# Performance work log

Measured on AMD Instinct MI355X. Metric: run time of the kernel, lower is better.

The kernel has to match this reference:

```python
import jax, jax.numpy as jnp
import numpy as np

B, S, SEG, D = 2, 128, 128, 768
RL, H, DK = 16, 8, 64
DV = D // H            # 96, dim_value = dim // heads
NRPF = D // H          # num_rel_pos_features
N = S * RL             # 2048 attention tokens
SCALE = DK ** -0.5


def setup_inputs() -> dict:
    key = jax.random.key(0)
    ks = jax.random.split(key, 12)
    g = lambda k, sh: jax.random.normal(k, sh, jnp.float32) * 0.02
    return {
        'x': jax.random.normal(ks[0], (B, S, SEG, D), jnp.float32),
        'ln_g': jnp.ones((D,), jnp.float32),
        'ln_b': jnp.zeros((D,), jnp.float32),
        'Wq': g(ks[1], (D, H * DK)),
        'Wk': g(ks[2], (D, H * DK)),
        'Wv': g(ks[3], (D, H * DV)),
        'Wr': g(ks[4], (NRPF, H * DK)),
        'r_w_bias': g(ks[5], (H, DK)),
        'r_r_bias': g(ks[6], (H, DK)),
        'Wo': g(ks[7], (H * DV, D)),
        'bo': jnp.zeros((D,), jnp.float32),
        'pos_emb': g(ks[8], (2 * N - 1, NRPF)),  # relative position features, dist -(N-1)..(N-1)
    }


def _layernorm(x, g, b, eps=1e-5):
    mu = jnp.mean(x, -1, keepdims=True)
    var = jnp.var(x, -1, keepdims=True)
    return (x - mu) * jax.lax.rsqrt(var + eps) * g + b


def _relative_shift(t):
    # t: [b, h, n, 2n-1] -> [b, h, n, n] (enformer-style shift)
    b, h, n, _ = t.shape
    t = jnp.pad(t, ((0, 0), (0, 0), (0, 0), (1, 0)))      # [b,h,n,2n]
    t = t.reshape(b, h, 2 * n, n)[:, :, 1:, :]            # [b,h,2n-1,n]
    t = t.reshape(b, h, n, 2 * n - 1)
    return t[..., :n]


def reference(x, ln_g, ln_b, Wq, Wk, Wv, Wr, r_w_bias, r_r_bias, Wo, bo, pos_emb):
    # slice representative tokens per segment and flatten: b s n d -> b (s n) d
    reps = x[:, :, :RL, :].reshape(B, N, D)
    h = _layernorm(reps, ln_g, ln_b)
    q = (h @ Wq).reshape(B, N, H, DK).transpose(0, 2, 1, 3) * SCALE  # bhnd
    k = (h @ Wk).reshape(B, N, H, DK).transpose(0, 2, 1, 3)
    v = (h @ Wv).reshape(B, N, H, DV).transpose(0, 2, 1, 3)
    content = jnp.einsum('bhid,bhjd->bhij', q + r_w_bias[None, :, None, :], k)
    rel_k = (pos_emb @ Wr).reshape(2 * N - 1, H, DK)
    rel = jnp.einsum('bhid,rhd->bhir', q + r_r_bias[None, :, None, :], rel_k)
    logits = content + _relative_shift(rel)
    attn = jax.nn.softmax(logits, axis=-1)
    out = jnp.einsum('bhij,bhjd->bhid', attn, v)
    out = out.transpose(0, 2, 1, 3).reshape(B, N, H * DV) @ Wo + bo
    reps = (reps + out).reshape(B, S, RL, D)  # residual transformer block, un-flatten
    return jnp.concatenate([reps, x[:, :, RL:, :]], axis=2)
```

## Files before the change

kernel.cpp:

```cpp
#include <hip/hip_runtime.h>

typedef short s8v __attribute__((ext_vector_type(8)));
typedef float f4 __attribute__((ext_vector_type(4)));

__device__ inline float bf2f(unsigned short u) {
  union { unsigned i; float f; } x; x.i = (unsigned)u << 16; return x.f;
}
__device__ inline unsigned short f2bf(float f) {
  union { float f; unsigned i; } x; x.f = f;
  return (unsigned short)((x.i + 0x7fffu + ((x.i >> 16) & 1u)) >> 16);
}

__device__ inline void gload16(const void* g, void* l) {
  __builtin_amdgcn_global_load_lds(
      (const __attribute__((address_space(1))) unsigned int*)g,
      (__attribute__((address_space(3))) unsigned int*)l, 16, 0, 0);
}

__device__ inline void bar_lgkm() {
  asm volatile("s_waitcnt lgkmcnt(0)" ::: "memory");
  __builtin_amdgcn_s_barrier();
  asm volatile("" ::: "memory");
}

__global__ __launch_bounds__(256) void copy4(const float4* __restrict__ src,
                                             float4* __restrict__ dst, int n4) {
  int i = blockIdx.x * blockDim.x + threadIdx.x;
  int stride = gridDim.x * blockDim.x;
  for (; i < n4; i += stride) dst[i] = src[i];
}

__global__ __launch_bounds__(256) void ln_kernel(const float* __restrict__ x,
                                                 const float* __restrict__ g,
                                                 const float* __restrict__ bvec,
                                                 unsigned short* __restrict__ h) {
  int m = blockIdx.x;
  int b = m >> 11, n = m & 2047;
  int s = n >> 4, rl = n & 15;
  const float* row = x + ((size_t)((b * 128 + s) * 128 + rl)) * 768;
  int t = threadIdx.x;
  float v0 = row[t], v1 = row[t + 256], v2 = row[t + 512];
  float sum = v0 + v1 + v2;
  float sq = v0 * v0 + v1 * v1 + v2 * v2;
  __shared__ float rs[4], rq[4];
#pragma unroll
  for (int o = 32; o; o >>= 1) {
    sum += __shfl_down(sum, o);
    sq += __shfl_down(sq, o);
  }
  if ((t & 63) == 0) { rs[t >> 6] = sum; rq[t >> 6] = sq; }
  __syncthreads();
  sum = rs[0] + rs[1] + rs[2] + rs[3];
  sq = rq[0] + rq[1] + rq[2] + rq[3];
  float mu = sum * (1.f / 768.f);
  float var = sq * (1.f / 768.f) - mu * mu;
  float inv = rsqrtf(var + 1e-5f);
  unsigned short* hrow = h + (size_t)m * 768;
  hrow[t] = f2bf((v0 - mu) * inv * g[t] + bvec[t]);
  hrow[t + 256] = f2bf((v1 - mu) * inv * g[t + 256] + bvec[t + 256]);
  hrow[t + 512] = f2bf((v2 - mu) * inv * g[t + 512] + bvec[t + 512]);
}

__global__ __launch_bounds__(256) void transp_cvt(const float* __restrict__ Wq,
                                                  const float* __restrict__ Wk,
                                                  const float* __restrict__ Wv,
                                                  const float* __restrict__ Wo,
                                                  unsigned short* __restrict__ Bt,
                                                  unsigned short* __restrict__ Bto) {
  int z = blockIdx.z;
  const float* src; unsigned short* dst; int N;
  if (z == 0) { src = Wq; dst = Bt; N = 512; }
  else if (z == 1) { src = Wk; dst = Bt + (size_t)512 * 768; N = 512; }
  else if (z == 2) { src = Wv; dst = Bt + (size_t)1024 * 768; N = 768; }
  else { src = Wo; dst = Bto; N = 768; }
  int n0 = blockIdx.x << 6, k0 = blockIdx.y << 6;
  if (n0 >= N) return;
  __shared__ float tile[64][65];
  int t = threadIdx.x;
  int c4 = (t & 15) << 2, rr = t >> 4;
#pragma unroll
  for (int i = 0; i < 4; ++i) {
    int kr = rr + (i << 4);
    float4 v = *(const float4*)(src + (size_t)(k0 + kr) * N + n0 + c4);
    tile[c4 + 0][kr] = v.x; tile[c4 + 1][kr] = v.y;
    tile[c4 + 2][kr] = v.z; tile[c4 + 3][kr] = v.w;
  }
  __syncthreads();
  int rowN = t >> 2, kc = (t & 3) << 4;
#pragma unroll
  for (int j = 0; j < 16; ++j)
    dst[(size_t)(n0 + rowN) * 768 + k0 + kc + j] = f2bf(tile[rowN][kc + j]);
}

__global__ __launch_bounds__(256) void gemm_rel(const float* __restrict__ A,
                                                const float* __restrict__ Bw,
                                                unsigned short* __restrict__ C0,
                                                int M, int Nn, int K) {
  __shared__ float As[16][68];
  __shared__ float Bs[16][68];
  int t = threadIdx.x;
  int tx = t & 15, ty = t >> 4;
  int row0 = blockIdx.y << 6, col0 = blockIdx.x << 6;
  float acc[4][4] = {{0.f}};
  int ar = t >> 2, ac = (t & 3) << 2;
  int br = t >> 4, bc = (t & 15) << 2;
  for (int k0 = 0; k0 < K; k0 += 16) {
    float4 av = make_float4(0.f, 0.f, 0.f, 0.f);
    if (row0 + ar < M) av = *(const float4*)(A + (size_t)(row0 + ar) * K + k0 + ac);
    As[ac + 0][ar] = av.x; As[ac + 1][ar] = av.y;
    As[ac + 2][ar] = av.z; As[ac + 3][ar] = av.w;
    float4 bv = *(const float4*)(Bw + (size_t)(k0 + br) * Nn + col0 + bc);
    *(float4*)&Bs[br][bc] = bv;
    __syncthreads();
#pragma unroll
    for (int kk = 0; kk < 16; ++kk) {
      float4 a = *(const float4*)&As[kk][ty << 2];
      float4 b = *(const float4*)&Bs[kk][tx << 2];
      float arr[4] = {a.x, a.y, a.z, a.w};
      float brr[4] = {b.x, b.y, b.z, b.w};
#pragma unroll
      for (int i = 0; i < 4; ++i)
#pragma unroll
        for (int j = 0; j < 4; ++j) acc[i][j] += arr[i] * brr[j];
    }
    __syncthreads();
  }
#pragma unroll
  for (int i = 0; i < 4; ++i) {
    int r = row0 + (ty << 2) + i;
    if (r >= M) continue;
    int colb = col0 + (tx << 2);
    unsigned pk0 = f2bf(acc[i][0]) | ((unsigned)f2bf(acc[i][1]) << 16);
    unsigned pk1 = f2bf(acc[i][2]) | ((unsigned)f2bf(acc[i][3]) << 16);
    *(uint2*)(C0 + (size_t)r * Nn + colb) = make_uint2(pk0, pk1);
  }
}

template <int MODE>
__global__ __launch_bounds__(256) void gemm_mfma(
    const unsigned short* __restrict__ A, const unsigned short* __restrict__ Bt,
    unsigned short* __restrict__ qw, unsigned short* __restrict__ qr,
    unsigned short* __restrict__ kbuf, unsigned short* __restrict__ vt,
    const float* __restrict__ rwb, const float* __restrict__ rrb,
    const float* __restrict__ x, const float* __restrict__ bo,
    float* __restrict__ out) {
  __shared__ __align__(16) short As[128 * 64];
  __shared__ __align__(16) short Bs[128 * 64];
  const int t = threadIdx.x;
  const int w = t >> 6, lane = t & 63;
  const int m16 = lane & 15, quad = lane >> 4;
  const int wm = w >> 1, wn = w & 1;
  const int m0 = blockIdx.y << 7, n0 = blockIdx.x << 7;
  const int K = 768;

  f4 acc[4][4];
#pragma unroll
  for (int i = 0; i < 4; ++i)
#pragma unroll
    for (int j = 0; j < 4; ++j) acc[i][j] = (f4){0.f, 0.f, 0.f, 0.f};

  const int rA = lane >> 3;
  const int cA = lane & 7;

  for (int k0 = 0; k0 < K; k0 += 64) {
    __syncthreads();
#pragma unroll
    for (int i = 0; i < 4; ++i) {
      int seg = (w << 2) + i;
      int r = (seg << 3) + rA;
      int cg = cA ^ (r & 7);
      gload16(A + (size_t)(m0 + r) * K + k0 + (cg << 3), (short*)As + (seg << 9));
      gload16(Bt + (size_t)(n0 + r) * K + k0 + (cg << 3), (short*)Bs + (seg << 9));
    }
    __syncthreads();
#pragma unroll
    for (int kb = 0; kb < 2; ++kb) {
      int cs = ((kb << 2) + quad) ^ (m16 & 7);
      s8v af[4], bf[4];
#pragma unroll
      for (int mt = 0; mt < 4; ++mt) {
        int r = (wm << 6) + (mt << 4) + m16;
        af[mt] = *(const s8v*)(As + (r << 6) + (cs << 3));
      }
#pragma unroll
      for (int nt = 0; nt < 4; ++nt) {
        int rn = (wn << 6) + (nt << 4) + m16;
        bf[nt] = *(const s8v*)(Bs + (rn << 6) + (cs << 3));
      }
#pragma unroll
      for (int mt = 0; mt < 4; ++mt)
#pragma unroll
        for (int nt = 0; nt < 4; ++nt)
          acc[mt][nt] = __builtin_amdgcn_mfma_f32_16x16x32_bf16(af[mt], bf[nt], acc[mt][nt], 0, 0, 0);
    }
  }

#pragma unroll
  for (int nt = 0; nt < 4; ++nt) {
    int n = n0 + (wn << 6) + (nt << 4) + m16;
#pragma unroll
    for (int mt = 0; mt < 4; ++mt) {
#pragma unroll
      for (int rr = 0; rr < 4; ++rr) {
        int m = m0 + (wm << 6) + (mt << 4) + (quad << 2) + rr;
        float v = acc[mt][nt][rr];
        if (MODE == 0) {
          if (n < 512) {
            float vs = v * 0.125f;
            qw[(size_t)m * 512 + n] = f2bf(vs + rwb[n]);
            qr[(size_t)m * 512 + n] = f2bf(vs + rrb[n]);
          } else if (n < 1024) {
            kbuf[(size_t)m * 512 + (n - 512)] = f2bf(v);
          } else {
            int col = n - 1024;
            int b = m >> 11, j = m & 2047;
            vt[(((size_t)(b * 768 + col)) << 11) + j] = f2bf(v);
          }
        } else {
          int b = m >> 11, nn2 = m & 2047;
          int s = nn2 >> 4, rl = nn2 & 15;
          size_t base = ((size_t)((b * 128 + s) * 128 + rl)) * 768;
          out[base + n] = x[base + n] + v + bo[n];
        }
      }
    }
  }
}

__global__ __launch_bounds__(256) void attn_kernel(
    const unsigned short* __restrict__ qw_g, const unsigned short* __restrict__ qr_g,
    const unsigned short* __restrict__ k_g, const unsigned short* __restrict__ vt_g,
    const unsigned short* __restrict__ rk_g, unsigned short* __restrict__ ao) {
  const int qt = blockIdx.x, hh = blockIdx.y, b = blockIdx.z;
  const int i0 = qt << 5;
  const int t = threadIdx.x;
  const int lane = t & 63, w = t >> 6;
  const int m16 = lane & 15, quad = lane >> 4;
  const int mi = w & 1, njb = w >> 1;
  const int sr = t >> 3, sg = t & 7;

  __shared__ __align__(16) short qw_s[32 * 64];
  __shared__ __align__(16) short qr_s[32 * 64];
  __shared__ __align__(16) short k_s[2][64 * 64];
  __shared__ __align__(16) short rk_s[2][96 * 64];
  __shared__ __align__(16) short pb_s[32 * 64];
  __shared__ float p_s[32][68];
  __shared__ short t_s[32][104];
  __shared__ float alpha_s[32];
  __shared__ float linv_s[32];

  for (int u = t; u < 512; u += 256) {
    int tile = u >> 8, idx = u & 255, r = idx >> 3, ch = idx & 7;
    const unsigned short* src =
        (tile ? qr_g : qw_g) + (((size_t)(b * 2048 + i0 + r)) << 9) + (hh << 6) + (ch << 3);
    int4 vdat = *(const int4*)src;
    short* dst = (tile ? qr_s : qw_s) + r * 64 + (((ch ^ (r & 7))) << 3);
    *(int4*)dst = vdat;
  }

  {
    const int rb0 = 2016 - i0;
#pragma unroll
    for (int s = 0; s < 2; ++s) {
      int slot = w * 2 + s;
      int u = (slot << 6) + lane;
      int r = u >> 3, c = u & 7;
      int cg = c ^ (r & 7);
      gload16(k_g + (((size_t)(b * 2048 + r)) << 9) + (hh << 6) + (cg << 3),
              (short*)k_s[0] + (slot << 9));
    }
#pragma unroll
    for (int s = 0; s < 3; ++s) {
      int slot = w * 3 + s;
      int u = (slot << 6) + lane;
      int r = u >> 3, c = u & 7;
      int cg = c ^ (r & 7);
      int grow = rb0 + r; if (grow > 4094) grow = 4094;
      gload16(rk_g + (((size_t)grow) << 9) + (hh << 6) + (cg << 3),
              (short*)rk_s[0] + (slot << 9));
    }
  }
  __syncthreads();

  float m_i = -1e30f, l_i = 0.f;
  f4 o0 = {0.f, 0.f, 0.f, 0.f}, o1 = o0, o2 = o0;
  const int arow = mi * 16 + m16;
  const int asw = arow & 7;
  const int crow = mi * 16 + quad * 4;
  const int brow0 = njb * 16 + m16;
  const int bsw = brow0 & 7;

  const unsigned short* vbase = vt_g + (((size_t)(b * 768 + hh * 96 + brow0)) << 11);

  for (int j0 = 0; j0 < 2048; j0 += 64) {
    const int cur = (j0 >> 6) & 1;

    const unsigned short* vb = vbase + j0;
    s8v va0 = *(const s8v*)(vb + (quad << 3));
    s8v va1 = *(const s8v*)(vb + 65536 + (quad << 3));
    s8v va2 = *(const s8v*)(vb + 131072 + (quad << 3));
    s8v vc0 = *(const s8v*)(vb + ((4 + quad) << 3));
    s8v vc1 = *(const s8v*)(vb + 65536 + ((4 + quad) << 3));
    s8v vc2 = *(const s8v*)(vb + 131072 + ((4 + quad) << 3));

    if (j0 < 1984) {
      const int j0n = j0 + 64;
      const int rbn = 2016 + j0n - i0;
#pragma unroll
      for (int s = 0; s < 2; ++s) {
        int slot = w * 2 + s;
        int u = (slot << 6) + lane;
        int r = u >> 3, c = u & 7;
        int cg = c ^ (r & 7);
        gload16(k_g + (((size_t)(b * 2048 + j0n + r)) << 9) + (hh << 6) + (cg << 3),
                (short*)k_s[cur ^ 1] + (slot << 9));
      }
#pragma unroll
      for (int s = 0; s < 3; ++s) {
        int slot = w * 3 + s;
        int u = (slot << 6) + lane;
        int r = u >> 3, c = u & 7;
        int cg = c ^ (r & 7);
        int grow = rbn + r; if (grow > 4094) grow = 4094;
        gload16(rk_g + (((size_t)grow) << 9) + (hh << 6) + (cg << 3),
                (short*)rk_s[cur ^ 1] + (slot << 9));
      }
    }

    if (j0 < 1984) asm volatile("s_waitcnt vmcnt(11)" ::: "memory");
    else           asm volatile("s_waitcnt vmcnt(6)" ::: "memory");
    __builtin_amdgcn_sched_barrier(0);

    const short* ks = k_s[cur];
    const short* rs = rk_s[cur];
    f4 c0 = {0.f, 0.f, 0.f, 0.f}, c1 = c0;
    f4 r0 = c0, r1 = c0, r2 = c0;
#pragma unroll
    for (int kb = 0; kb < 2; ++kb) {
      const int cidx = (kb << 2) + quad;
      const int co = (cidx ^ asw) << 3;
      const int cb = (cidx ^ bsw) << 3;
      s8v aq = *(const s8v*)(qw_s + arow * 64 + co);
      s8v ar = *(const s8v*)(qr_s + arow * 64 + co);
      s8v bk0 = *(const s8v*)(ks + brow0 * 64 + cb);
      s8v bk1 = *(const s8v*)(ks + (brow0 + 32) * 64 + cb);
      s8v br0 = *(const s8v*)(rs + brow0 * 64 + cb);
      s8v br1 = *(const s8v*)(rs + (brow0 + 32) * 64 + cb);
      s8v br2 = *(const s8v*)(rs + (brow0 + 64) * 64 + cb);
      __builtin_amdgcn_s_setprio(1);
      c0 = __builtin_amdgcn_mfma_f32_16x16x32_bf16(aq, bk0, c0, 0, 0, 0);
      c1 = __builtin_amdgcn_mfma_f32_16x16x32_bf16(aq, bk1, c1, 0, 0, 0);
      r0 = __builtin_amdgcn_mfma_f32_16x16x32_bf16(ar, br0, r0, 0, 0, 0);
      r1 = __builtin_amdgcn_mfma_f32_16x16x32_bf16(ar, br1, r1, 0, 0, 0);
      r2 = __builtin_amdgcn_mfma_f32_16x16x32_bf16(ar, br2, r2, 0, 0, 0);
      __builtin_amdgcn_s_setprio(0);
    }
#pragma unroll
    for (int rr = 0; rr < 4; ++rr) {
      p_s[crow + rr][njb * 16 + m16] = c0[rr];
      p_s[crow + rr][(njb + 2) * 16 + m16] = c1[rr];
      t_s[crow + rr][njb * 16 + m16] = (short)f2bf(r0[rr]);
      t_s[crow + rr][(njb + 2) * 16 + m16] = (short)f2bf(r1[rr]);
      t_s[crow + rr][(njb + 4) * 16 + m16] = (short)f2bf(r2[rr]);
    }
    bar_lgkm();

    float sv[8];
    float mx = -1e30f;
#pragma unroll
    for (int j2 = 0; j2 < 8; ++j2) {
      int c = sg + (j2 << 3);
      float s = p_s[sr][c] + bf2f((unsigned short)t_s[sr][c - sr + 31]);
      sv[j2] = s;
      mx = fmaxf(mx, s);
    }
    mx = fmaxf(mx, __shfl_xor(mx, 1));
    mx = fmaxf(mx, __shfl_xor(mx, 2));
    mx = fmaxf(mx, __shfl_xor(mx, 4));
    float m_new = fmaxf(m_i, mx);
    float al = __expf(m_i - m_new);
    float sm = 0.f;
#pragma unroll
    for (int j2 = 0; j2 < 8; ++j2) {
      float p = __expf(sv[j2] - m_new);
      sm += p;
      pb_s[sr * 64 + ((j2 ^ (sr & 7)) << 3) + sg] = (short)f2bf(p);
    }
    sm += __shfl_xor(sm, 1);
    sm += __shfl_xor(sm, 2);
    sm += __shfl_xor(sm, 4);
    l_i = l_i * al + sm;
    m_i = m_new;
    if (sg == 0) alpha_s[sr] = al;
    bar_lgkm();

#pragma unroll
    for (int rr = 0; rr < 4; ++rr) {
      float a = alpha_s[crow + rr];
      o0[rr] *= a; o1[rr] *= a; o2[rr] *= a;
    }
#pragma unroll
    for (int kb = 0; kb < 2; ++kb) {
      const int cidx = (kb << 2) + quad;
      const int co = (cidx ^ asw) << 3;
      s8v ap = *(const s8v*)(pb_s + arow * 64 + co);
      s8v b0v = kb ? vc0 : va0;
      s8v b1v = kb ? vc1 : va1;
      s8v b2v = kb ? vc2 : va2;
      __builtin_amdgcn_s_setprio(1);
      o0 = __builtin_amdgcn_mfma_f32_16x16x32_bf16(ap, b0v, o0, 0, 0, 0);
      o1 = __builtin_amdgcn_mfma_f32_16x16x32_bf16(ap, b1v, o1, 0, 0, 0);
      o2 = __builtin_amdgcn_mfma_f32_16x16x32_bf16(ap, b2v, o2, 0, 0, 0);
      __builtin_amdgcn_s_setprio(0);
    }
  }

  if (sg == 0) linv_s[sr] = 1.f / l_i;
  __syncthreads();
#pragma unroll
  for (int rr = 0; rr < 4; ++rr) {
    int row = crow + rr;
    float inv = linv_s[row];
    size_t gbase = ((size_t)(b * 2048 + i0 + row)) * 768 + hh * 96;
    ao[gbase + njb * 16 + m16] = f2bf(o0[rr] * inv);
    ao[gbase + (njb + 2) * 16 + m16] = f2bf(o1[rr] * inv);
    ao[gbase + (njb + 4) * 16 + m16] = f2bf(o2[rr] * inv);
  }
}

extern "C" void kernel_launch(void* const* d_in, const int* in_sizes, int n_in,
                              void* d_out, int out_size, void* d_ws, size_t ws_size,
                              hipStream_t stream) {
  (void)in_sizes; (void)n_in; (void)out_size; (void)ws_size;
  const float* x = (const float*)d_in[0];
  const float* ln_g = (const float*)d_in[1];
  const float* ln_b = (const float*)d_in[2];
  const float* Wq = (const float*)d_in[3];
  const float* Wk = (const float*)d_in[4];
  const float* Wv = (const float*)d_in[5];
  const float* Wr = (const float*)d_in[6];
  const float* rwb = (const float*)d_in[7];
  const float* rrb = (const float*)d_in[8];
  const float* Wo = (const float*)d_in[9];
  const float* bo = (const float*)d_in[10];
  const float* pe = (const float*)d_in[11];
  float* out = (float*)d_out;

  char* p = (char*)d_ws;
  unsigned short* hbf = (unsigned short*)p; p += (size_t)4096 * 768 * 2;
  unsigned short* qw = (unsigned short*)p;  p += (size_t)4096 * 512 * 2;
  unsigned short* qr = (unsigned short*)p;  p += (size_t)4096 * 512 * 2;
  unsigned short* kb = (unsigned short*)p;  p += (size_t)4096 * 512 * 2;
  unsigned short* vt = (unsigned short*)p;  p += (size_t)4096 * 768 * 2;
  unsigned short* rk = (unsigned short*)p;  p += (size_t)4095 * 512 * 2;
  unsigned short* ao = (unsigned short*)p;  p += (size_t)4096 * 768 * 2;
  unsigned short* Bt = (unsigned short*)p;  p += (size_t)1792 * 768 * 2;
  unsigned short* Bto = (unsigned short*)p;

  transp_cvt<<<dim3(12, 12, 4), dim3(256), 0, stream>>>(Wq, Wk, Wv, Wo, Bt, Bto);
  copy4<<<dim3(2048), dim3(256), 0, stream>>>((const float4*)x, (float4*)out, 6291456);
  ln_kernel<<<dim3(4096), dim3(256), 0, stream>>>(x, ln_g, ln_b, hbf);
  gemm_rel<<<dim3(8, 64), dim3(256), 0, stream>>>(pe, Wr, rk, 4095, 512, 96);
  gemm_mfma<0><<<dim3(14, 32), dim3(256), 0, stream>>>(hbf, Bt, qw, qr, kb, vt, rwb, rrb,
                                                       nullptr, nullptr, nullptr);
  attn_kernel<<<dim3(64, 8, 2), dim3(256), 0, stream>>>(qw, qr, kb, vt, rk, ao);
  gemm_mfma<1><<<dim3(6, 32), dim3(256), 0, stream>>>(ao, Bto, nullptr, nullptr, nullptr,
                                                      nullptr, nullptr, nullptr, x, bo, out);
}
```

Before: 410.0 us.

## Fuse output copy into attention kernel and keep rel-pos keys in registers

Removes the standalone copy kernel and spreads the x-to-out copy across the first 24 iterations of the attention loop, so memory traffic overlaps MFMA work. Relative-position key fragments are now loaded directly from global memory into registers, with a one-iteration prefetch, instead of being staged in LDS. This cuts shared memory use, and occupancy is requested at 3 blocks per SM. The tradeoffs are higher register pressure, global loads that are not coalesced through LDS, and a hand-tuned vmcnt wait that must stay correct.

```diff
diff --git a/kernel.cpp b/kernel.cpp
--- a/kernel.cpp
+++ b/kernel.cpp
@@ -21,13 +21,6 @@
   asm volatile("s_waitcnt lgkmcnt(0)" ::: "memory");
   __builtin_amdgcn_s_barrier();
   asm volatile("" ::: "memory");
-}
-
-__global__ __launch_bounds__(256) void copy4(const float4* __restrict__ src,
-                                             float4* __restrict__ dst, int n4) {
-  int i = blockIdx.x * blockDim.x + threadIdx.x;
-  int stride = gridDim.x * blockDim.x;
-  for (; i < n4; i += stride) dst[i] = src[i];
 }
 
 __global__ __launch_bounds__(256) void ln_kernel(const float* __restrict__ x,
@@ -227,10 +220,11 @@
   }
 }
 
-__global__ __launch_bounds__(256) void attn_kernel(
+__global__ __launch_bounds__(256, 3) void attn_kernel(
     const unsigned short* __restrict__ qw_g, const unsigned short* __restrict__ qr_g,
     const unsigned short* __restrict__ k_g, const unsigned short* __restrict__ vt_g,
-    const unsigned short* __restrict__ rk_g, unsigned short* __restrict__ ao) {
+    const unsigned short* __restrict__ rk_g, unsigned short* __restrict__ ao,
+    const float4* __restrict__ xc, float4* __restrict__ outc) {
   const int qt = blockIdx.x, hh = blockIdx.y, b = blockIdx.z;
   const int i0 = qt << 5;
   const int t = threadIdx.x;
@@ -238,16 +232,22 @@
   const int m16 = lane & 15, quad = lane >> 4;
   const int mi = w & 1, njb = w >> 1;
   const int sr = t >> 3, sg = t & 7;
+  const int bid = qt + (hh << 6) + (b << 9);
 
   __shared__ __align__(16) short qw_s[32 * 64];
   __shared__ __align__(16) short qr_s[32 * 64];
   __shared__ __align__(16) short k_s[2][64 * 64];
-  __shared__ __align__(16) short rk_s[2][96 * 64];
   __shared__ __align__(16) short pb_s[32 * 64];
   __shared__ float p_s[32][68];
   __shared__ short t_s[32][104];
   __shared__ float alpha_s[32];
   __shared__ float linv_s[32];
+
+  const int arow = mi * 16 + m16;
+  const int asw = arow & 7;
+  const int crow = mi * 16 + quad * 4;
+  const int brow0 = njb * 16 + m16;
+  const int bsw = brow0 & 7;
 
   for (int u = t; u < 512; u += 256) {
     int tile = u >> 8, idx = u & 255, r = idx >> 3, ch = idx & 7;
@@ -258,39 +258,39 @@
     *(int4*)dst = vdat;
   }
 
+#pragma unroll
+  for (int s = 0; s < 2; ++s) {
+    int slot = w * 2 + s;
+    int u = (slot << 6) + lane;
+    int r = u >> 3, c = u & 7;
+    int cg = c ^ (r & 7);
+    gload16(k_g + (((size_t)(b * 2048 + r)) << 9) + (hh << 6) + (cg << 3),
+            (short*)k_s[0] + (slot << 9));
+  }
+
+  const unsigned short* rk_h = rk_g + (hh << 6);
+  const int rb0 = 2016 - i0;
+  s8v cr0a, cr0b, cr1a, cr1b, cr2a, cr2b;
   {
-    const int rb0 = 2016 - i0;
-#pragma unroll
-    for (int s = 0; s < 2; ++s) {
-      int slot = w * 2 + s;
-      int u = (slot << 6) + lane;
-      int r = u >> 3, c = u & 7;
-      int cg = c ^ (r & 7);
-      gload16(k_g + (((size_t)(b * 2048 + r)) << 9) + (hh << 6) + (cg << 3),
-              (short*)k_s[0] + (slot << 9));
-    }
-#pragma unroll
-    for (int s = 0; s < 3; ++s) {
-      int slot = w * 3 + s;
-      int u = (slot << 6) + lane;
-      int r = u >> 3, c = u & 7;
-      int cg = c ^ (r & 7);
-      int grow = rb0 + r; if (grow > 4094) grow = 4094;
-      gload16(rk_g + (((size_t)grow) << 9) + (hh << 6) + (cg << 3),
-              (short*)rk_s[0] + (slot << 9));
-    }
+    int g0 = rb0 + brow0, g1 = g0 + 32, g2 = g0 + 64;
+    if (g2 > 4094) g2 = 4094;
+    const unsigned short* p0 = rk_h + ((size_t)g0 << 9);
+    const unsigned short* p1 = rk_h + ((size_t)g1 << 9);
+    const unsigned short* p2 = rk_h + ((size_t)g2 << 9);
+    cr0a = *(const s8v*)(p0 + (quad << 3));
+    cr0b = *(const s8v*)(p0 + ((4 + quad) << 3));
+    cr1a = *(const s8v*)(p1 + (quad << 3));
+    cr1b = *(const s8v*)(p1 + ((4 + quad) << 3));
+    cr2a = *(const s8v*)(p2 + (quad << 3));
+    cr2b = *(const s8v*)(p2 + ((4 + quad) << 3));
   }
   __syncthreads();
 
   float m_i = -1e30f, l_i = 0.f;
   f4 o0 = {0.f, 0.f, 0.f, 0.f}, o1 = o0, o2 = o0;
-  const int arow = mi * 16 + m16;
-  const int asw = arow & 7;
-  const int crow = mi * 16 + quad * 4;
-  const int brow0 = njb * 16 + m16;
-  const int bsw = brow0 & 7;
-
   const unsigned short* vbase = vt_g + (((size_t)(b * 768 + hh * 96 + brow0)) << 11);
+
+  s8v nr0a = cr0a, nr0b = cr0b, nr1a = cr1a, nr1b = cr1b, nr2a = cr2a, nr2b = cr2b;
 
   for (int j0 = 0; j0 < 2048; j0 += 64) {
     const int cur = (j0 >> 6) & 1;
@@ -305,7 +305,6 @@
 
     if (j0 < 1984) {
       const int j0n = j0 + 64;
-      const int rbn = 2016 + j0n - i0;
 #pragma unroll
       for (int s = 0; s < 2; ++s) {
         int slot = w * 2 + s;
@@ -315,24 +314,18 @@
         gload16(k_g + (((size_t)(b * 2048 + j0n + r)) << 9) + (hh << 6) + (cg << 3),
                 (short*)k_s[cur ^ 1] + (slot << 9));
       }
-#pragma unroll
-      for (int s = 0; s < 3; ++s) {
-        int slot = w * 3 + s;
-        int u = (slot << 6) + lane;
-        int r = u >> 3, c = u & 7;
-        int cg = c ^ (r & 7);
-        int grow = rbn + r; if (grow > 4094) grow = 4094;
-        gload16(rk_g + (((size_t)grow) << 9) + (hh << 6) + (cg << 3),
-                (short*)rk_s[cur ^ 1] + (slot << 9));
-      }
-    }
-
-    if (j0 < 1984) asm volatile("s_waitcnt vmcnt(11)" ::: "memory");
-    else           asm volatile("s_waitcnt vmcnt(6)" ::: "memory");
+    }
+
+    asm volatile("s_waitcnt vmcnt(8)" ::: "memory");
     __builtin_amdgcn_sched_barrier(0);
 
-    const short* ks = k_s[cur];
-    const short* rs = rk_s[cur];
+    const int it = j0 >> 6;
+    const bool do_copy = it < 24;
+    const int cix = (((it << 10) + bid) << 8) + t;
+    float4 cval;
+    if (do_copy) cval = xc[(size_t)cix];
+
+    const short* ks = (const short*)k_s[cur];
     f4 c0 = {0.f, 0.f, 0.f, 0.f}, c1 = c0;
     f4 r0 = c0, r1 = c0, r2 = c0;
 #pragma unroll
@@ -344,9 +337,9 @@
       s8v ar = *(const s8v*)(qr_s + arow * 64 + co);
       s8v bk0 = *(const s8v*)(ks + brow0 * 64 + cb);
       s8v bk1 = *(const s8v*)(ks + (brow0 + 32) * 64 + cb);
-      s8v br0 = *(const s8v*)(rs + brow0 * 64 + cb);
-      s8v br1 = *(const s8v*)(rs + (brow0 + 32) * 64 + cb);
-      s8v br2 = *(const s8v*)(rs + (brow0 + 64) * 64 + cb);
+      s8v br0 = kb ? cr0b : cr0a;
+      s8v br1 = kb ? cr1b : cr1a;
+      s8v br2 = kb ? cr2b : cr2a;
       __builtin_amdgcn_s_setprio(1);
       c0 = __builtin_amdgcn_mfma_f32_16x16x32_bf16(aq, bk0, c0, 0, 0, 0);
       c1 = __builtin_amdgcn_mfma_f32_16x16x32_bf16(aq, bk1, c1, 0, 0, 0);
@@ -355,6 +348,22 @@
       r2 = __builtin_amdgcn_mfma_f32_16x16x32_bf16(ar, br2, r2, 0, 0, 0);
       __builtin_amdgcn_s_setprio(0);
     }
+
+    if (j0 < 1984) {
+      const int rbn = rb0 + j0 + 64;
+      int g0 = rbn + brow0, g1 = g0 + 32, g2 = g0 + 64;
+      if (g2 > 4094) g2 = 4094;
+      const unsigned short* p0 = rk_h + ((size_t)g0 << 9);
+      const unsigned short* p1 = rk_h + ((size_t)g1 << 9);
+      const unsigned short* p2 = rk_h + ((size_t)g2 << 9);
+      nr0a = *(const s8v*)(p0 + (quad << 3));
+      nr0b = *(const s8v*)(p0 + ((4 + quad) << 3));
+      nr1a = *(const s8v*)(p1 + (quad << 3));
+      nr1b = *(const s8v*)(p1 + ((4 + quad) << 3));
+      nr2a = *(const s8v*)(p2 + (quad << 3));
+      nr2b = *(const s8v*)(p2 + ((4 + quad) << 3));
+    }
+
 #pragma unroll
     for (int rr = 0; rr < 4; ++rr) {
       p_s[crow + rr][njb * 16 + m16] = c0[rr];
@@ -393,6 +402,8 @@
     m_i = m_new;
     if (sg == 0) alpha_s[sr] = al;
     bar_lgkm();
+
+    if (do_copy) outc[(size_t)cix] = cval;
 
 #pragma unroll
     for (int rr = 0; rr < 4; ++rr) {
@@ -412,6 +423,12 @@
       o1 = __builtin_amdgcn_mfma_f32_16x16x32_bf16(ap, b1v, o1, 0, 0, 0);
       o2 = __builtin_amdgcn_mfma_f32_16x16x32_bf16(ap, b2v, o2, 0, 0, 0);
       __builtin_amdgcn_s_setprio(0);
+    }
+
+    if (j0 < 1984) {
+      cr0a = nr0a; cr0b = nr0b;
+      cr1a = nr1a; cr1b = nr1b;
+      cr2a = nr2a; cr2b = nr2b;
     }
   }
 
@@ -458,12 +475,12 @@
   unsigned short* Bto = (unsigned short*)p;
 
   transp_cvt<<<dim3(12, 12, 4), dim3(256), 0, stream>>>(Wq, Wk, Wv, Wo, Bt, Bto);
-  copy4<<<dim3(2048), dim3(256), 0, stream>>>((const float4*)x, (float4*)out, 6291456);
   ln_kernel<<<dim3(4096), dim3(256), 0, stream>>>(x, ln_g, ln_b, hbf);
   gemm_rel<<<dim3(8, 64), dim3(256), 0, stream>>>(pe, Wr, rk, 4095, 512, 96);
   gemm_mfma<0><<<dim3(14, 32), dim3(256), 0, stream>>>(hbf, Bt, qw, qr, kb, vt, rwb, rrb,
                                                        nullptr, nullptr, nullptr);
-  attn_kernel<<<dim3(64, 8, 2), dim3(256), 0, stream>>>(qw, qr, kb, vt, rk, ao);
+  attn_kernel<<<dim3(64, 8, 2), dim3(256), 0, stream>>>(qw, qr, kb, vt, rk, ao,
+                                                        (const float4*)x, (float4*)out);
   gemm_mfma<1><<<dim3(6, 32), dim3(256), 0, stream>>>(ao, Bto, nullptr, nullptr, nullptr,
                                                       nullptr, nullptr, nullptr, x, bo, out);
 }
```

Result: slower. 445.0 us (+8.5%).
